# Performance work log

Hardware: AMD Instinct MI355X
Metric: run time of the kernel (lower is better)

## Reference

```python
import jax, jax.numpy as jnp
import numpy as np

B, D, H, S, REP, OUT = 4096, 256, 256, 3, 10, 44


def setup_inputs():
    key = jax.random.key(0)
    ks = jax.random.split(key, 30)
    def rn(k, shape, scale=1.0):
        return jax.random.normal(k, shape, dtype=jnp.float32) * scale
    w = 0.05
    return {
        "x": rn(ks[0], (B, D)),
        "hidden0": rn(ks[1], (S, B, H)),
        "current0": rn(ks[2], (S, B, H)),
        "Wi_f": rn(ks[3], (S, H, D), w), "bi_f": rn(ks[4], (S, H), w),
        "Wi_i": rn(ks[5], (S, H, D), w), "bi_i": rn(ks[6], (S, H), w),
        "Wi_o": rn(ks[7], (S, H, D), w), "bi_o": rn(ks[8], (S, H), w),
        "Wi_c": rn(ks[9], (S, H, D), w), "bi_c": rn(ks[10], (S, H), w),
        "Wi_g": rn(ks[11], (S, S, D), w), "bi_g": rn(ks[12], (S, S), w),
        "Wh_f": rn(ks[13], (S, H, H), w), "bh_f": rn(ks[14], (S, H), w),
        "Wh_i": rn(ks[15], (S, H, H), w), "bh_i": rn(ks[16], (S, H), w),
        "Wh_o": rn(ks[17], (S, H, H), w), "bh_o": rn(ks[18], (S, H), w),
        "Wh_g": rn(ks[19], (S, S, S * H), w), "bh_g": rn(ks[20], (S, S), w),
        "Wh_c": rn(ks[21], (S, S * H, S * H), w), "bh_c": rn(ks[22], (S, S * H), w),
        "W_last": rn(ks[23], (OUT, (REP - 1) * H), w), "b_last": rn(ks[24], (OUT,), w),
    }


def _lin(x, W, b):
    return x @ W.T + b


def _gflstm(x, hidden0, current0, Wi_f, bi_f, Wi_i, bi_i, Wi_o, bi_o, Wi_c, bi_c,
            Wi_g, bi_g, Wh_f, bh_f, Wh_i, bh_i, Wh_o, bh_o, Wh_g, bh_g,
            Wh_c, bh_c, W_last, b_last):
    S_, B_, H_ = hidden0.shape
    rep = W_last.shape[1] // H_ + 1  # (rep_time-1)*H in-features of last layer
    h_prev, c_prev = hidden0, current0
    last_layer_hs = []
    for t in range(rep):  # fixed small trip-count, sequential recurrence
        # torch.cat(hidden[t], 1): layer-major concat -> [B, S*H]
        h_cat = jnp.transpose(h_prev, (1, 0, 2)).reshape(B_, S_ * H_)
        input_h = x
        h_list, c_list = [], []
        for l in range(S_):
            f = jax.nn.sigmoid(_lin(input_h, Wi_f[l], bi_f[l]) + _lin(h_prev[l], Wh_f[l], bh_f[l]))
            i = jax.nn.sigmoid(_lin(input_h, Wi_i[l], bi_i[l]) + _lin(h_prev[l], Wh_i[l], bh_i[l]))
            g = jax.nn.sigmoid(_lin(input_h, Wi_g[l], bi_g[l]) + _lin(h_cat, Wh_g[l], bh_g[l]))  # [B, S]
            aux = _lin(h_cat, Wh_c[l], bh_c[l]).reshape(B_, S_, H_)
            aux = (aux * g[:, :, None]).sum(axis=1)  # gated cross-layer weighted sum -> [B, H]
            c_t = jnp.tanh(_lin(input_h, Wi_c[l], bi_c[l]) + aux)
            c = f * c_prev[l] + i * c_t
            o = jax.nn.sigmoid(_lin(input_h, Wi_o[l], bi_o[l]) + _lin(h_prev[l], Wh_o[l], bh_o[l]))
            h = o * c
            input_h = h
            h_list.append(h)
            c_list.append(c)
        h_prev = jnp.stack(h_list)
        c_prev = jnp.stack(c_list)
        if t < rep - 1:  # output uses hidden[1..rep-1][-1]
            last_layer_hs.append(h_list[-1])
    feat = jnp.concatenate(last_layer_hs, axis=1)  # [B, (rep-1)*H]
    return jax.nn.sigmoid(_lin(feat, W_last, b_last))


def reference(x, hidden0, current0, Wi_f, bi_f, Wi_i, bi_i, Wi_o, bi_o, Wi_c, bi_c,
              Wi_g, bi_g, Wh_f, bh_f, Wh_i, bh_i, Wh_o, bh_o, Wh_g, bh_g,
              Wh_c, bh_c, W_last, b_last):
    return _gflstm(x, hidden0, current0, Wi_f, bi_f, Wi_i, bi_i, Wi_o, bi_o, Wi_c, bi_c,
                   Wi_g, bi_g, Wh_f, bh_f, Wh_i, bh_i, Wh_o, bh_o, Wh_g, bh_g,
                   Wh_c, bh_c, W_last, b_last)
```

## Files before the change

kernel.cpp:

```cpp
#include <hip/hip_runtime.h>
#include <hip/hip_bf16.h>

typedef __hip_bfloat16 bf16;
typedef __attribute__((ext_vector_type(8))) short frag8;
typedef __attribute__((ext_vector_type(4))) float f32x4;

#define BM 128
#define BN 128
#define BK 64
#define SK 72

__device__ __forceinline__ float sigm(float x) { return 1.f / (1.f + __expf(-x)); }

__device__ __forceinline__ void lds_load16(const bf16* g, short* l) {
    __builtin_amdgcn_global_load_lds(
        (const __attribute__((address_space(1))) void*)g,
        (__attribute__((address_space(3))) void*)l, 16, 0, 0);
}

__global__ __launch_bounds__(256, 2)
void gemm_bt(const bf16* __restrict__ A, int lda, long long sAz,
             const bf16* __restrict__ W, int ldw, long long sWz,
             void* __restrict__ Cv, int ldc, long long sCz, int K,
             int outmode, const float* __restrict__ bias, int nbound)
{
    __shared__ short As[BM * SK];
    __shared__ short Bs[BN * SK];
    const int z = blockIdx.z;
    A += (size_t)z * sAz;
    W += (size_t)z * sWz;
    const int m0 = blockIdx.y * BM;
    const int n0 = blockIdx.x * BN;
    const int tid  = threadIdx.x;
    const int lane = tid & 63;
    const int wave = tid >> 6;
    const int wm = (wave >> 1) * 64;
    const int wn = (wave & 1) * 64;
    const int q   = lane >> 4;
    const int r16 = lane & 15;

    f32x4 acc[4][4] = {};

    const int trow = tid >> 3;
    const int tcol = (tid & 7) * 8;

    for (int k0 = 0; k0 < K; k0 += BK) {
        __syncthreads();
        #pragma unroll
        for (int p = 0; p < 4; ++p) {
            int rr = p * 32 + trow;
            *(uint4*)&As[rr * SK + tcol] =
                *(const uint4*)(A + (size_t)(m0 + rr) * lda + k0 + tcol);
            *(uint4*)&Bs[rr * SK + tcol] =
                *(const uint4*)(W + (size_t)(n0 + rr) * ldw + k0 + tcol);
        }
        __syncthreads();
        #pragma unroll
        for (int kk = 0; kk < 2; ++kk) {
            const int ko = kk * 32 + q * 8;
            frag8 af[4], bfr[4];
            #pragma unroll
            for (int i = 0; i < 4; ++i)
                af[i] = *(const frag8*)&As[(wm + i * 16 + r16) * SK + ko];
            #pragma unroll
            for (int j = 0; j < 4; ++j)
                bfr[j] = *(const frag8*)&Bs[(wn + j * 16 + r16) * SK + ko];
            #pragma unroll
            for (int i = 0; i < 4; ++i)
                #pragma unroll
                for (int j = 0; j < 4; ++j)
                    acc[i][j] = __builtin_amdgcn_mfma_f32_16x16x32_bf16(
                        af[i], bfr[j], acc[i][j], 0, 0, 0);
        }
    }

    if (outmode == 0) {
        float* C = (float*)Cv + (size_t)z * sCz;
        #pragma unroll
        for (int i = 0; i < 4; ++i)
            #pragma unroll
            for (int rr = 0; rr < 4; ++rr) {
                int row = m0 + wm + i * 16 + q * 4 + rr;
                float* crow = C + (size_t)row * ldc + n0 + wn + r16;
                #pragma unroll
                for (int j = 0; j < 4; ++j) crow[j * 16] = acc[i][j][rr];
            }
    } else if (outmode == 1) {
        bf16* C = (bf16*)Cv + (size_t)z * sCz;
        #pragma unroll
        for (int i = 0; i < 4; ++i)
            #pragma unroll
            for (int rr = 0; rr < 4; ++rr) {
                int row = m0 + wm + i * 16 + q * 4 + rr;
                bf16* crow = C + (size_t)row * ldc + n0 + wn + r16;
                #pragma unroll
                for (int j = 0; j < 4; ++j) crow[j * 16] = __float2bfloat16(acc[i][j][rr]);
            }
    } else if (outmode == 2) {
        float* C = (float*)Cv + (size_t)z * sCz;
        #pragma unroll
        for (int i = 0; i < 4; ++i)
            #pragma unroll
            for (int rr = 0; rr < 4; ++rr) {
                int row = m0 + wm + i * 16 + q * 4 + rr;
                #pragma unroll
                for (int j = 0; j < 4; ++j) {
                    int col = n0 + wn + j * 16 + r16;
                    if (col < nbound)
                        C[(size_t)row * ldc + col] = sigm(acc[i][j][rr] + bias[col]);
                }
            }
    } else {
        float* C = (float*)Cv + (size_t)z * sCz;
        #pragma unroll
        for (int i = 0; i < 4; ++i)
            #pragma unroll
            for (int rr = 0; rr < 4; ++rr) {
                int row = m0 + wm + i * 16 + q * 4 + rr;
                #pragma unroll
                for (int j = 0; j < 4; ++j) {
                    int col = n0 + wn + j * 16 + r16;
                    if (col < nbound)
                        C[(size_t)row * ldc + col] = acc[i][j][rr];
                }
            }
    }
}

__global__ __launch_bounds__(256, 3)
void gemm_hidden(const bf16* __restrict__ hprev,
                 const bf16* __restrict__ WhFIO,
                 const bf16* __restrict__ WhCb,
                 const bf16* __restrict__ WgH,
                 const float* __restrict__ big, const float* __restrict__ bhg,
                 bf16* __restrict__ hgb,
                 bf16* __restrict__ auxb,
                 float* __restrict__ gh)
{
    __shared__ __align__(16) short As[BM * 64];
    __shared__ __align__(16) short Bs[BN * 64];
    __shared__ __align__(16) short Bg[16 * 64];

    const int zi = blockIdx.x % 6;
    const int xt = blockIdx.x / 6;
    const bool isaux = zi >= 3;
    const int l = isaux ? zi - 3 : zi;
    const bf16* A = hprev + (isaux ? 0 : l * 256);
    const int K = isaux ? 768 : 256;
    const bf16* W = isaux ? (WhCb + (size_t)l * 768 * 768) : (WhFIO + (size_t)l * 768 * 256);
    const int ldw = isaux ? 768 : 256;
    bf16* C = (isaux ? auxb : hgb) + (size_t)l * 4096 * 768;
    const bool do_g = isaux && (xt == 0);

    const int m0 = blockIdx.y * BM;
    const int n0 = xt * BN;
    const int tid  = threadIdx.x;
    const int lane = tid & 63;
    const int wave = tid >> 6;
    const int wm = (wave >> 1) * 64;
    const int wn = (wave & 1) * 64;
    const int q   = lane >> 4;
    const int r16 = lane & 15;

    f32x4 acc[4][4] = {};
    f32x4 accg[4] = {};

    const int srow = lane >> 3;
    const int scolsw = ((lane & 7) ^ srow) * 8;
    const bf16* WgL = WgH + (size_t)l * 16 * 768;

    for (int k0 = 0; k0 < K; k0 += BK) {
        __syncthreads();
        #pragma unroll
        for (int p = 0; p < 4; ++p) {
            int rbase = (wave * 4 + p) * 8;
            lds_load16(A + (size_t)(m0 + rbase + srow) * 768 + k0 + scolsw, &As[rbase * 64]);
            lds_load16(W + (size_t)(n0 + rbase + srow) * ldw + k0 + scolsw, &Bs[rbase * 64]);
        }
        if (do_g && wave < 2)
            lds_load16(WgL + (size_t)(wave * 8 + srow) * 768 + k0 + scolsw, &Bg[wave * 8 * 64]);
        __syncthreads();
        #pragma unroll
        for (int kk = 0; kk < 2; ++kk) {
            const int c = kk * 4 + q;
            frag8 af[4], bfr[4];
            #pragma unroll
            for (int i = 0; i < 4; ++i) {
                int R = wm + i * 16 + r16;
                af[i] = *(const frag8*)&As[R * 64 + ((c ^ (R & 7)) << 3)];
            }
            #pragma unroll
            for (int j = 0; j < 4; ++j) {
                int R = wn + j * 16 + r16;
                bfr[j] = *(const frag8*)&Bs[R * 64 + ((c ^ (R & 7)) << 3)];
            }
            #pragma unroll
            for (int i = 0; i < 4; ++i)
                #pragma unroll
                for (int j = 0; j < 4; ++j)
                    acc[i][j] = __builtin_amdgcn_mfma_f32_16x16x32_bf16(
                        af[i], bfr[j], acc[i][j], 0, 0, 0);
            if (do_g) {
                frag8 bg = *(const frag8*)&Bg[r16 * 64 + ((c ^ (r16 & 7)) << 3)];
                #pragma unroll
                for (int i = 0; i < 4; ++i)
                    accg[i] = __builtin_amdgcn_mfma_f32_16x16x32_bf16(
                        af[i], bg, accg[i], 0, 0, 0);
            }
        }
    }

    #pragma unroll
    for (int i = 0; i < 4; ++i)
        #pragma unroll
        for (int rr = 0; rr < 4; ++rr) {
            int row = m0 + wm + i * 16 + q * 4 + rr;
            bf16* crow = C + (size_t)row * 768 + n0 + wn + r16;
            #pragma unroll
            for (int j = 0; j < 4; ++j) crow[j * 16] = __float2bfloat16(acc[i][j][rr]);
        }
    if (do_g && wn == 0 && r16 < 3) {
        float bsum = big[l * 3 + r16] + bhg[l * 3 + r16];
        #pragma unroll
        for (int i = 0; i < 4; ++i)
            #pragma unroll
            for (int rr = 0; rr < 4; ++rr) {
                int row = m0 + wm + i * 16 + q * 4 + rr;
                gh[(size_t)row * 9 + l * 3 + r16] = accg[i][rr] + bsum;
            }
    }
}

#define GM 64
struct Stage { short As[GM * 64]; short Bs[BN * 64]; short Bg[16 * 64]; };
union SMemU { Stage s; float ct[GM * 128]; };

__global__ __launch_bounds__(256, 2)
void gemm_gates(const bf16* __restrict__ A, int lda,
                const bf16* __restrict__ Wi, const bf16* __restrict__ Wg,
                const bf16* __restrict__ hg_l,
                const bf16* __restrict__ aux_l,
                const float* __restrict__ ghc_l,
                const float* __restrict__ cprev,
                const float* __restrict__ bif, const float* __restrict__ bhf,
                const float* __restrict__ bii, const float* __restrict__ bhi,
                const float* __restrict__ bio, const float* __restrict__ bho,
                const float* __restrict__ bic, const float* __restrict__ bhc,
                bf16*  __restrict__ hnew,
                float* __restrict__ cnew,
                bf16*  __restrict__ featc)
{
    __shared__ __align__(16) SMemU sm;
    __shared__ float gsh[GM * 3];

    const int m0 = blockIdx.y * GM;
    const int n0 = blockIdx.x * BN;
    const int jbase = n0 >> 2;
    const int tid  = threadIdx.x;
    const int lane = tid & 63;
    const int wave = tid >> 6;
    const int wm = (wave >> 1) * 32;
    const int wn = (wave & 1) * 64;
    const int q   = lane >> 4;
    const int r16 = lane & 15;

    f32x4 acc[2][4] = {};
    f32x4 accg[2] = {};

    const int srow = lane >> 3;
    const int scolsw = ((lane & 7) ^ srow) * 8;

    for (int k0 = 0; k0 < 256; k0 += BK) {
        __syncthreads();
        #pragma unroll
        for (int p = 0; p < 2; ++p) {
            int rbase = (wave * 2 + p) * 8;
            lds_load16(A + (size_t)(m0 + rbase + srow) * lda + k0 + scolsw, &sm.s.As[rbase * 64]);
        }
        #pragma unroll
        for (int p = 0; p < 4; ++p) {
            int rbase = (wave * 4 + p) * 8;
            lds_load16(Wi + (size_t)(n0 + rbase + srow) * 256 + k0 + scolsw, &sm.s.Bs[rbase * 64]);
        }
        if (wave < 2)
            lds_load16(Wg + (size_t)(wave * 8 + srow) * 256 + k0 + scolsw, &sm.s.Bg[wave * 8 * 64]);
        __syncthreads();
        #pragma unroll
        for (int kk = 0; kk < 2; ++kk) {
            const int c = kk * 4 + q;
            frag8 af[2], bfr[4], bg;
            bg = *(const frag8*)&sm.s.Bg[r16 * 64 + ((c ^ (r16 & 7)) << 3)];
            #pragma unroll
            for (int i = 0; i < 2; ++i) {
                int R = wm + i * 16 + r16;
                af[i] = *(const frag8*)&sm.s.As[R * 64 + ((c ^ (R & 7)) << 3)];
            }
            #pragma unroll
            for (int j = 0; j < 4; ++j) {
                int R = wn + j * 16 + r16;
                bfr[j] = *(const frag8*)&sm.s.Bs[R * 64 + ((c ^ (R & 7)) << 3)];
            }
            #pragma unroll
            for (int i = 0; i < 2; ++i) {
                #pragma unroll
                for (int j = 0; j < 4; ++j)
                    acc[i][j] = __builtin_amdgcn_mfma_f32_16x16x32_bf16(
                        af[i], bfr[j], acc[i][j], 0, 0, 0);
                accg[i] = __builtin_amdgcn_mfma_f32_16x16x32_bf16(
                    af[i], bg, accg[i], 0, 0, 0);
            }
        }
    }

    __syncthreads();
    if (wn == 0 && r16 < 3) {
        #pragma unroll
        for (int i = 0; i < 2; ++i)
            #pragma unroll
            for (int rr = 0; rr < 4; ++rr) {
                int row = wm + i * 16 + q * 4 + rr;
                gsh[row * 3 + r16] = sigm(accg[i][rr] + ghc_l[(size_t)(m0 + row) * 9 + r16]);
            }
    }
    #pragma unroll
    for (int i = 0; i < 2; ++i)
        #pragma unroll
        for (int rr = 0; rr < 4; ++rr) {
            int rowl = wm + i * 16 + q * 4 + rr;
            #pragma unroll
            for (int jr = 0; jr < 4; ++jr) {
                int col = wn + jr * 16 + r16;
                sm.ct[rowl * 128 + ((col + 4 * rowl) & 127)] = acc[i][jr][rr];
            }
        }
    __syncthreads();

    const int jj = tid & 31;
    const int r0 = (tid >> 5) * 8;
    const int j  = jbase + jj;
    const float vbif = bif[j], vbhf = bhf[j];
    const float vbii = bii[j], vbhi = bhi[j];
    const float vbio = bio[j], vbho = bho[j];
    const float vbic = bic[j];
    const float vbc0 = bhc[j], vbc1 = bhc[256 + j], vbc2 = bhc[512 + j];

    for (int ri = 0; ri < 8; ++ri) {
        int rowl = r0 + ri;
        size_t b = m0 + rowl;
        float4 pre = *(float4*)&sm.ct[rowl * 128 + ((4 * jj + 4 * rowl) & 127)];
        float g0 = gsh[rowl * 3 + 0];
        float g1 = gsh[rowl * 3 + 1];
        float g2 = gsh[rowl * 3 + 2];
        float hgf = __bfloat162float(hg_l[b * 768 + j]);
        float hgi = __bfloat162float(hg_l[b * 768 + 256 + j]);
        float hgo = __bfloat162float(hg_l[b * 768 + 512 + j]);
        float ax0 = __bfloat162float(aux_l[b * 768 + j]);
        float ax1 = __bfloat162float(aux_l[b * 768 + 256 + j]);
        float ax2 = __bfloat162float(aux_l[b * 768 + 512 + j]);
        float f  = sigm(pre.x + vbif + hgf + vbhf);
        float ii = sigm(pre.y + vbii + hgi + vbhi);
        float o  = sigm(pre.z + vbio + hgo + vbho);
        float av = g0 * (ax0 + vbc0) + g1 * (ax1 + vbc1) + g2 * (ax2 + vbc2);
        float ct = tanhf(pre.w + vbic + av);
        float c  = f * cprev[b * 256 + j] + ii * ct;
        float h  = o * c;
        cnew[b * 256 + j] = c;
        hnew[b * 768 + j] = __float2bfloat16(h);
        if (featc) featc[b * 2304 + j] = __float2bfloat16(h);
    }
}

__global__ __launch_bounds__(256)
void gates_pre(const bf16* __restrict__ ipre0i, const float* __restrict__ gin0,
               const float* __restrict__ ghc,
               const bf16* __restrict__ hg_l, const bf16* __restrict__ aux_l,
               const float* __restrict__ cprev,
               const float* __restrict__ bif, const float* __restrict__ bhf,
               const float* __restrict__ bii, const float* __restrict__ bhi,
               const float* __restrict__ bio, const float* __restrict__ bho,
               const float* __restrict__ bic, const float* __restrict__ bhc,
               bf16* __restrict__ hnew, float* __restrict__ cnew)
{
    const int j = threadIdx.x;
    const int b0 = blockIdx.x * 4;
    const float vbif = bif[j], vbhf = bhf[j];
    const float vbii = bii[j], vbhi = bhi[j];
    const float vbio = bio[j], vbho = bho[j];
    const float vbic = bic[j];
    const float vbc0 = bhc[j], vbc1 = bhc[256 + j], vbc2 = bhc[512 + j];

    #pragma unroll
    for (int r = 0; r < 4; ++r) {
        const size_t b = b0 + r;
        const bf16* ip4 = ipre0i + b * 1024 + 4 * j;
        float pf = __bfloat162float(ip4[0]);
        float pi = __bfloat162float(ip4[1]);
        float po = __bfloat162float(ip4[2]);
        float pc = __bfloat162float(ip4[3]);
        float g0 = sigm(gin0[b * 3 + 0] + ghc[b * 9 + 0]);
        float g1 = sigm(gin0[b * 3 + 1] + ghc[b * 9 + 1]);
        float g2 = sigm(gin0[b * 3 + 2] + ghc[b * 9 + 2]);
        float hgf = __bfloat162float(hg_l[b * 768 + j]);
        float hgi = __bfloat162float(hg_l[b * 768 + 256 + j]);
        float hgo = __bfloat162float(hg_l[b * 768 + 512 + j]);
        float ax0 = __bfloat162float(aux_l[b * 768 + j]);
        float ax1 = __bfloat162float(aux_l[b * 768 + 256 + j]);
        float ax2 = __bfloat162float(aux_l[b * 768 + 512 + j]);
        float f  = sigm(pf + vbif + hgf + vbhf);
        float ii = sigm(pi + vbii + hgi + vbhi);
        float o  = sigm(po + vbio + hgo + vbho);
        float av = g0 * (ax0 + vbc0) + g1 * (ax1 + vbc1) + g2 * (ax2 + vbc2);
        float ct = tanhf(pc + vbic + av);
        float c  = f * cprev[b * 256 + j] + ii * ct;
        float h  = o * c;
        cnew[b * 256 + j] = c;
        hnew[b * 768 + j] = __float2bfloat16(h);
    }
}

__global__ __launch_bounds__(256)
void gin0_kernel(const bf16* __restrict__ xb, const float* __restrict__ Wig,
                 float* __restrict__ gout)
{
    const int wave = threadIdx.x >> 6, lane = threadIdx.x & 63;
    for (int rep = 0; rep < 4; ++rep) {
        size_t b = (size_t)blockIdx.x * 16 + wave * 4 + rep;
        float hv[4];
        #pragma unroll
        for (int m = 0; m < 4; ++m)
            hv[m] = __bfloat162float(xb[b * 256 + m * 64 + lane]);
        float p[3];
        #pragma unroll
        for (int s = 0; s < 3; ++s) {
            float t = 0.f;
            const float* w = Wig + (size_t)s * 256;
            #pragma unroll
            for (int m = 0; m < 4; ++m) t += hv[m] * w[m * 64 + lane];
            p[s] = t;
        }
        #pragma unroll
        for (int off = 32; off; off >>= 1)
            #pragma unroll
            for (int s = 0; s < 3; ++s) p[s] += __shfl_down(p[s], off);
        if (lane == 0) {
            #pragma unroll
            for (int s = 0; s < 3; ++s) gout[b * 3 + s] = p[s];
        }
    }
}

__global__ __launch_bounds__(256)
void final_reduce(const float* __restrict__ part, const float* __restrict__ bl,
                  float* __restrict__ out)
{
    int idx = blockIdx.x * 256 + threadIdx.x;
    if (idx >= 4096 * 44) return;
    int b = idx / 44, n = idx - b * 44;
    float s = bl[n];
    #pragma unroll
    for (int z = 0; z < 12; ++z) s += part[(size_t)z * 4096 * 64 + (size_t)b * 64 + n];
    out[idx] = sigm(s);
}

__global__ __launch_bounds__(256)
void prep_all(const float* __restrict__ Wi_f, const float* __restrict__ Wi_i,
              const float* __restrict__ Wi_o, const float* __restrict__ Wi_c,
              const float* __restrict__ Wh_f, const float* __restrict__ Wh_i,
              const float* __restrict__ Wh_o, const float* __restrict__ Wh_c,
              const float* __restrict__ Wi_g, const float* __restrict__ Wh_g,
              const float* __restrict__ W_last, const float* __restrict__ x,
              const float* __restrict__ hidden0, const float* __restrict__ current0,
              bf16* __restrict__ WiCatI, bf16* __restrict__ WhFIO,
              bf16* __restrict__ WhCb, bf16* __restrict__ Wgb,
              bf16* __restrict__ WgH, bf16* __restrict__ Wlb,
              bf16* __restrict__ xb, bf16* __restrict__ hcat, float* __restrict__ c0)
{
    int idx = blockIdx.x * 256 + threadIdx.x;
    if (idx < 786432) {
        int k = idx & 255, n = (idx >> 8) & 1023, l = idx >> 18;
        int j = n >> 2, g = n & 3;
        const float* src = (g == 0) ? Wi_f : (g == 1) ? Wi_i : (g == 2) ? Wi_o : Wi_c;
        WiCatI[idx] = __float2bfloat16(src[l * 65536 + j * 256 + k]);
        return;
    }
    idx -= 786432;
    if (idx < 589824) {
        int k = idx & 255, n = (idx >> 8) % 768, l = idx / 196608;
        const float* src = (n < 256) ? Wh_f : (n < 512) ? Wh_i : Wh_o;
        WhFIO[idx] = __float2bfloat16(src[l * 65536 + (n & 255) * 256 + k]);
        return;
    }
    idx -= 589824;
    if (idx < 1769472) {
        WhCb[idx] = __float2bfloat16(Wh_c[idx]);
        return;
    }
    idx -= 1769472;
    if (idx < 12288) {
        int k = idx & 255, r = (idx >> 8) & 15, l = idx >> 12;
        Wgb[idx] = (r < 3) ? __float2bfloat16(Wi_g[l * 768 + r * 256 + k])
                           : __float2bfloat16(0.f);
        return;
    }
    idx -= 12288;
    if (idx < 36864) {
        int k = idx % 768, r = (idx / 768) & 15, l = idx / (16 * 768);
        WgH[idx] = (r < 3) ? __float2bfloat16(Wh_g[(l * 3 + r) * 768 + k])
                           : __float2bfloat16(0.f);
        return;
    }
    idx -= 36864;
    if (idx < 294912) {
        int k = idx % 2304, n = idx / 2304;
        Wlb[idx] = (n < 44) ? __float2bfloat16(W_last[n * 2304 + k])
                            : __float2bfloat16(0.f);
        return;
    }
    idx -= 294912;
    if (idx < 1048576) {
        xb[idx] = __float2bfloat16(x[idx]);
        return;
    }
    idx -= 1048576;
    if (idx < 3145728) {
        int j = idx & 255, b = (idx >> 8) & 4095, l = idx >> 20;
        hcat[(size_t)b * 768 + l * 256 + j] = __float2bfloat16(hidden0[idx]);
        c0[idx] = current0[idx];
    }
}

extern "C" void kernel_launch(void* const* d_in, const int* in_sizes, int n_in,
                              void* d_out, int out_size, void* d_ws, size_t ws_size,
                              hipStream_t stream)
{
    (void)in_sizes; (void)n_in; (void)out_size; (void)ws_size;
    const float* x        = (const float*)d_in[0];
    const float* hidden0  = (const float*)d_in[1];
    const float* current0 = (const float*)d_in[2];
    const float* Wi_f = (const float*)d_in[3];  const float* bi_f = (const float*)d_in[4];
    const float* Wi_i = (const float*)d_in[5];  const float* bi_i = (const float*)d_in[6];
    const float* Wi_o = (const float*)d_in[7];  const float* bi_o = (const float*)d_in[8];
    const float* Wi_c = (const float*)d_in[9];  const float* bi_c = (const float*)d_in[10];
    const float* Wi_g = (const float*)d_in[11]; const float* bi_g = (const float*)d_in[12];
    const float* Wh_f = (const float*)d_in[13]; const float* bh_f = (const float*)d_in[14];
    const float* Wh_i = (const float*)d_in[15]; const float* bh_i = (const float*)d_in[16];
    const float* Wh_o = (const float*)d_in[17]; const float* bh_o = (const float*)d_in[18];
    const float* Wh_g = (const float*)d_in[19]; const float* bh_g = (const float*)d_in[20];
    const float* Wh_c = (const float*)d_in[21]; const float* bh_c = (const float*)d_in[22];
    const float* W_last = (const float*)d_in[23]; const float* b_last = (const float*)d_in[24];

    char* p = (char*)d_ws;
    bf16* WiCatI = (bf16*)p; p += (size_t)3 * 1024 * 256 * 2;
    bf16* WhFIO  = (bf16*)p; p += (size_t)3 * 768 * 256 * 2;
    bf16* WhCb   = (bf16*)p; p += (size_t)3 * 768 * 768 * 2;
    bf16* Wgb    = (bf16*)p; p += (size_t)3 * 16 * 256 * 2;
    bf16* WgH    = (bf16*)p; p += (size_t)3 * 16 * 768 * 2;
    bf16* Wlb    = (bf16*)p; p += (size_t)128 * 2304 * 2;
    bf16* xb     = (bf16*)p; p += (size_t)4096 * 256 * 2;
    bf16* ipre0i = (bf16*)p; p += (size_t)4096 * 1024 * 2;
    float* gin0  = (float*)p; p += (size_t)4096 * 3 * 4;
    bf16* hb0    = (bf16*)p; p += (size_t)4096 * 768 * 2;
    bf16* hb1    = (bf16*)p; p += (size_t)4096 * 768 * 2;
    float* cb0   = (float*)p; p += (size_t)3 * 4096 * 256 * 4;
    float* cb1   = (float*)p; p += (size_t)3 * 4096 * 256 * 4;
    bf16* hgb    = (bf16*)p; p += (size_t)3 * 4096 * 768 * 2;
    bf16* auxb   = (bf16*)p; p += (size_t)3 * 4096 * 768 * 2;
    float* gh    = (float*)p; p += (size_t)4096 * 9 * 4;
    bf16* feat   = (bf16*)p; p += (size_t)4096 * 2304 * 2;
    float* partf = (float*)p; p += (size_t)12 * 4096 * 64 * 4;

    prep_all<<<30017, 256, 0, stream>>>(
        Wi_f, Wi_i, Wi_o, Wi_c, Wh_f, Wh_i, Wh_o, Wh_c, Wi_g, Wh_g, W_last, x,
        hidden0, current0,
        WiCatI, WhFIO, WhCb, Wgb, WgH, Wlb, xb, hb0, cb0);

    gemm_bt<<<dim3(8, 32, 1), 256, 0, stream>>>(xb, 256, 0, WiCatI, 256, 0,
                                                ipre0i, 1024, 0, 256, 1, nullptr, 0);
    gin0_kernel<<<256, 256, 0, stream>>>(xb, Wi_g, gin0);

    for (int t = 0; t < 10; ++t) {
        bf16* hprev = (t & 1) ? hb1 : hb0;
        bf16* hnew  = (t & 1) ? hb0 : hb1;
        float* cprev = (t & 1) ? cb1 : cb0;
        float* cnew  = (t & 1) ? cb0 : cb1;

        gemm_hidden<<<dim3(36, 32), 256, 0, stream>>>(
            hprev, WhFIO, WhCb, WgH, bi_g, bh_g, hgb, auxb, gh);

        gates_pre<<<1024, 256, 0, stream>>>(
            ipre0i, gin0, gh,
            hgb, auxb, cprev,
            bi_f, bh_f, bi_i, bh_i, bi_o, bh_o, bi_c, bh_c,
            hnew, cnew);

        for (int l = 1; l < 3; ++l) {
            gemm_gates<<<dim3(8, 64), 256, 0, stream>>>(
                (const bf16*)(hnew + (l - 1) * 256), 768,
                WiCatI + (size_t)l * 1024 * 256,
                Wgb + (size_t)l * 16 * 256,
                hgb + (size_t)l * 4096 * 768,
                auxb + (size_t)l * 4096 * 768,
                gh + l * 3,
                cprev + (size_t)l * 4096 * 256,
                bi_f + l * 256, bh_f + l * 256,
                bi_i + l * 256, bh_i + l * 256,
                bi_o + l * 256, bh_o + l * 256,
                bi_c + l * 256, bh_c + l * 768,
                hnew + l * 256,
                cnew + (size_t)l * 4096 * 256,
                (l == 2 && t < 9) ? (feat + (size_t)t * 256) : (bf16*)nullptr);
        }
    }

    gemm_bt<<<dim3(1, 32, 12), 256, 0, stream>>>(
        feat, 2304, 192, Wlb, 2304, 192,
        partf, 64, (long long)4096 * 64, 192, 3, nullptr, 64);
    final_reduce<<<704, 256, 0, stream>>>(partf, b_last, (float*)d_out);
}
```

Measured before the change: 824.0 us.

## Halve gemm_gates row tile and fold input gate projection into initial GEMM

Drops the gemm_gates row tile from 64 to 32 rows, so each wave handles a single 16-row fragment and the grid doubles to 1024 blocks. This spreads the per-layer gate GEMM across more CUs and cuts registers per wave. It also removes the separate gin0 kernel by computing the x·Wi_g projection with extra MFMAs inside the first gemm_bt launch, using the bf16 Wg weights. The trade-off is lower MFMA reuse per B-tile load in gemm_gates, and gin0 now comes from bf16 rather than fp32 weights.

After: 782.9 us. 1.05x faster.

```diff
diff --git a/kernel.cpp b/kernel.cpp
--- a/kernel.cpp
+++ b/kernel.cpp
@@ -22,10 +22,12 @@
 void gemm_bt(const bf16* __restrict__ A, int lda, long long sAz,
              const bf16* __restrict__ W, int ldw, long long sWz,
              void* __restrict__ Cv, int ldc, long long sCz, int K,
-             int outmode, const float* __restrict__ bias, int nbound)
+             int outmode, const float* __restrict__ bias, int nbound,
+             const bf16* __restrict__ Wg, float* __restrict__ gout)
 {
     __shared__ short As[BM * SK];
     __shared__ short Bs[BN * SK];
+    __shared__ short Bg[16 * SK];
     const int z = blockIdx.z;
     A += (size_t)z * sAz;
     W += (size_t)z * sWz;
@@ -38,8 +40,10 @@
     const int wn = (wave & 1) * 64;
     const int q   = lane >> 4;
     const int r16 = lane & 15;
+    const bool do_g = (Wg != nullptr) && (blockIdx.x == 0);
 
     f32x4 acc[4][4] = {};
+    f32x4 accg[4] = {};
 
     const int trow = tid >> 3;
     const int tcol = (tid & 7) * 8;
@@ -54,6 +58,9 @@
             *(uint4*)&Bs[rr * SK + tcol] =
                 *(const uint4*)(W + (size_t)(n0 + rr) * ldw + k0 + tcol);
         }
+        if (do_g && tid < 128)
+            *(uint4*)&Bg[(tid >> 3) * SK + tcol] =
+                *(const uint4*)(Wg + (size_t)(tid >> 3) * 256 + k0 + tcol);
         __syncthreads();
         #pragma unroll
         for (int kk = 0; kk < 2; ++kk) {
@@ -71,6 +78,13 @@
                 for (int j = 0; j < 4; ++j)
                     acc[i][j] = __builtin_amdgcn_mfma_f32_16x16x32_bf16(
                         af[i], bfr[j], acc[i][j], 0, 0, 0);
+            if (do_g) {
+                frag8 bg = *(const frag8*)&Bg[r16 * SK + ko];
+                #pragma unroll
+                for (int i = 0; i < 4; ++i)
+                    accg[i] = __builtin_amdgcn_mfma_f32_16x16x32_bf16(
+                        af[i], bg, accg[i], 0, 0, 0);
+            }
         }
     }
 
@@ -123,6 +137,15 @@
                     if (col < nbound)
                         C[(size_t)row * ldc + col] = acc[i][j][rr];
                 }
+            }
+    }
+    if (do_g && wn == 0 && r16 < 3) {
+        #pragma unroll
+        for (int i = 0; i < 4; ++i)
+            #pragma unroll
+            for (int rr = 0; rr < 4; ++rr) {
+                int row = m0 + wm + i * 16 + q * 4 + rr;
+                gout[(size_t)row * 3 + r16] = accg[i][rr];
             }
     }
 }
@@ -231,7 +254,7 @@
     }
 }
 
-#define GM 64
+#define GM 32
 struct Stage { short As[GM * 64]; short Bs[BN * 64]; short Bg[16 * 64]; };
 union SMemU { Stage s; float ct[GM * 128]; };
 
@@ -259,24 +282,21 @@
     const int tid  = threadIdx.x;
     const int lane = tid & 63;
     const int wave = tid >> 6;
-    const int wm = (wave >> 1) * 32;
+    const int wm = (wave >> 1) * 16;
     const int wn = (wave & 1) * 64;
     const int q   = lane >> 4;
     const int r16 = lane & 15;
 
-    f32x4 acc[2][4] = {};
-    f32x4 accg[2] = {};
+    f32x4 acc[4] = {};
+    f32x4 accg = {};
 
     const int srow = lane >> 3;
     const int scolsw = ((lane & 7) ^ srow) * 8;
 
     for (int k0 = 0; k0 < 256; k0 += BK) {
         __syncthreads();
-        #pragma unroll
-        for (int p = 0; p < 2; ++p) {
-            int rbase = (wave * 2 + p) * 8;
-            lds_load16(A + (size_t)(m0 + rbase + srow) * lda + k0 + scolsw, &sm.s.As[rbase * 64]);
-        }
+        lds_load16(A + (size_t)(m0 + wave * 8 + srow) * lda + k0 + scolsw,
+                   &sm.s.As[wave * 8 * 64]);
         #pragma unroll
         for (int p = 0; p < 4; ++p) {
             int rbase = (wave * 4 + p) * 8;
@@ -288,12 +308,11 @@
         #pragma unroll
         for (int kk = 0; kk < 2; ++kk) {
             const int c = kk * 4 + q;
-            frag8 af[2], bfr[4], bg;
+            frag8 af, bfr[4], bg;
             bg = *(const frag8*)&sm.s.Bg[r16 * 64 + ((c ^ (r16 & 7)) << 3)];
-            #pragma unroll
-            for (int i = 0; i < 2; ++i) {
-                int R = wm + i * 16 + r16;
-                af[i] = *(const frag8*)&sm.s.As[R * 64 + ((c ^ (R & 7)) << 3)];
+            {
+                int R = wm + r16;
+                af = *(const frag8*)&sm.s.As[R * 64 + ((c ^ (R & 7)) << 3)];
             }
             #pragma unroll
             for (int j = 0; j < 4; ++j) {
@@ -301,42 +320,33 @@
                 bfr[j] = *(const frag8*)&sm.s.Bs[R * 64 + ((c ^ (R & 7)) << 3)];
             }
             #pragma unroll
-            for (int i = 0; i < 2; ++i) {
-                #pragma unroll
-                for (int j = 0; j < 4; ++j)
-                    acc[i][j] = __builtin_amdgcn_mfma_f32_16x16x32_bf16(
-                        af[i], bfr[j], acc[i][j], 0, 0, 0);
-                accg[i] = __builtin_amdgcn_mfma_f32_16x16x32_bf16(
-                    af[i], bg, accg[i], 0, 0, 0);
-            }
+            for (int j = 0; j < 4; ++j)
+                acc[j] = __builtin_amdgcn_mfma_f32_16x16x32_bf16(af, bfr[j], acc[j], 0, 0, 0);
+            accg = __builtin_amdgcn_mfma_f32_16x16x32_bf16(af, bg, accg, 0, 0, 0);
         }
     }
 
     __syncthreads();
     if (wn == 0 && r16 < 3) {
         #pragma unroll
-        for (int i = 0; i < 2; ++i)
-            #pragma unroll
-            for (int rr = 0; rr < 4; ++rr) {
-                int row = wm + i * 16 + q * 4 + rr;
-                gsh[row * 3 + r16] = sigm(accg[i][rr] + ghc_l[(size_t)(m0 + row) * 9 + r16]);
-            }
+        for (int rr = 0; rr < 4; ++rr) {
+            int row = wm + q * 4 + rr;
+            gsh[row * 3 + r16] = sigm(accg[rr] + ghc_l[(size_t)(m0 + row) * 9 + r16]);
+        }
     }
     #pragma unroll
-    for (int i = 0; i < 2; ++i)
-        #pragma unroll
-        for (int rr = 0; rr < 4; ++rr) {
-            int rowl = wm + i * 16 + q * 4 + rr;
-            #pragma unroll
-            for (int jr = 0; jr < 4; ++jr) {
-                int col = wn + jr * 16 + r16;
-                sm.ct[rowl * 128 + ((col + 4 * rowl) & 127)] = acc[i][jr][rr];
-            }
-        }
+    for (int rr = 0; rr < 4; ++rr) {
+        int rowl = wm + q * 4 + rr;
+        #pragma unroll
+        for (int jr = 0; jr < 4; ++jr) {
+            int col = wn + jr * 16 + r16;
+            sm.ct[rowl * 128 + ((col + 4 * rowl) & 127)] = acc[jr][rr];
+        }
+    }
     __syncthreads();
 
     const int jj = tid & 31;
-    const int r0 = (tid >> 5) * 8;
+    const int r0 = (tid >> 5) * 4;
     const int j  = jbase + jj;
     const float vbif = bif[j], vbhf = bhf[j];
     const float vbii = bii[j], vbhi = bhi[j];
@@ -344,7 +354,8 @@
     const float vbic = bic[j];
     const float vbc0 = bhc[j], vbc1 = bhc[256 + j], vbc2 = bhc[512 + j];
 
-    for (int ri = 0; ri < 8; ++ri) {
+    #pragma unroll
+    for (int ri = 0; ri < 4; ++ri) {
         int rowl = r0 + ri;
         size_t b = m0 + rowl;
         float4 pre = *(float4*)&sm.ct[rowl * 128 + ((4 * jj + 4 * rowl) & 127)];
@@ -419,37 +430,6 @@
 }
 
 __global__ __launch_bounds__(256)
-void gin0_kernel(const bf16* __restrict__ xb, const float* __restrict__ Wig,
-                 float* __restrict__ gout)
-{
-    const int wave = threadIdx.x >> 6, lane = threadIdx.x & 63;
-    for (int rep = 0; rep < 4; ++rep) {
-        size_t b = (size_t)blockIdx.x * 16 + wave * 4 + rep;
-        float hv[4];
-        #pragma unroll
-        for (int m = 0; m < 4; ++m)
-            hv[m] = __bfloat162float(xb[b * 256 + m * 64 + lane]);
-        float p[3];
-        #pragma unroll
-        for (int s = 0; s < 3; ++s) {
-            float t = 0.f;
-            const float* w = Wig + (size_t)s * 256;
-            #pragma unroll
-            for (int m = 0; m < 4; ++m) t += hv[m] * w[m * 64 + lane];
-            p[s] = t;
-        }
-        #pragma unroll
-        for (int off = 32; off; off >>= 1)
-            #pragma unroll
-            for (int s = 0; s < 3; ++s) p[s] += __shfl_down(p[s], off);
-        if (lane == 0) {
-            #pragma unroll
-            for (int s = 0; s < 3; ++s) gout[b * 3 + s] = p[s];
-        }
-    }
-}
-
-__global__ __launch_bounds__(256)
 void final_reduce(const float* __restrict__ part, const float* __restrict__ bl,
                   float* __restrict__ out)
 {
@@ -575,8 +555,8 @@
         WiCatI, WhFIO, WhCb, Wgb, WgH, Wlb, xb, hb0, cb0);
 
     gemm_bt<<<dim3(8, 32, 1), 256, 0, stream>>>(xb, 256, 0, WiCatI, 256, 0,
-                                                ipre0i, 1024, 0, 256, 1, nullptr, 0);
-    gin0_kernel<<<256, 256, 0, stream>>>(xb, Wi_g, gin0);
+                                                ipre0i, 1024, 0, 256, 1, nullptr, 0,
+                                                Wgb, gin0);
 
     for (int t = 0; t < 10; ++t) {
         bf16* hprev = (t & 1) ? hb1 : hb0;
@@ -594,7 +574,7 @@
             hnew, cnew);
 
         for (int l = 1; l < 3; ++l) {
-            gemm_gates<<<dim3(8, 64), 256, 0, stream>>>(
+            gemm_gates<<<dim3(8, 128), 256, 0, stream>>>(
                 (const bf16*)(hnew + (l - 1) * 256), 768,
                 WiCatI + (size_t)l * 1024 * 256,
                 Wgb + (size_t)l * 16 * 256,
@@ -614,6 +594,7 @@
 
     gemm_bt<<<dim3(1, 32, 12), 256, 0, stream>>>(
         feat, 2304, 192, Wlb, 2304, 192,
-        partf, 64, (long long)4096 * 64, 192, 3, nullptr, 64);
+        partf, 64, (long long)4096 * 64, 192, 3, nullptr, 64,
+        nullptr, nullptr);
     final_reduce<<<704, 256, 0, stream>>>(partf, b_last, (float*)d_out);
 }
```
